# Optimization experiments

Measured on AMD Instinct MI355X. Metric: run time of the kernel, lower is better.

Reference implementation:

```python
import jax, jax.numpy as jnp
import numpy as np


def _gru(x, h, Wx, Wh, b):
    # Keras-convention GRUCell (reset_after=False): h' = z*h + (1-z)*hh
    D = h.shape[-1]
    g = x @ Wx + b                       # [N, 3D]
    xz, xr, xh = g[..., :D], g[..., D:2 * D], g[..., 2 * D:]
    z = jax.nn.sigmoid(xz + h @ Wh[:, :D])
    r = jax.nn.sigmoid(xr + h @ Wh[:, D:2 * D])
    hh = jnp.tanh(xh + (r * h) @ Wh[:, 2 * D:])
    return z * h + (1.0 - z) * hh


def setup_inputs():
    key = jax.random.key(0)
    ks = jax.random.split(key, 12)
    num_links, num_quests, num_paths = 20000, 200, 100
    total_paths = num_quests * num_paths
    L, link_dim, path_dim, T = 8, 64, 64, 8
    s = 0.05
    links = jax.random.randint(ks[0], (total_paths * L,), 0, num_links)
    paths = jnp.repeat(jnp.arange(total_paths), L)   # sorted, as segment_sum requires
    seqs = jnp.tile(jnp.arange(L), total_paths)      # hop position within each path
    return {
        "link_capacity": jax.random.uniform(ks[1], (num_links,), jnp.float32),
        "traffic": jax.random.uniform(ks[2], (total_paths,), jnp.float32),
        "links": links, "paths": paths, "seqs": seqs,
        "pWx": jax.random.normal(ks[3], (link_dim, 3 * path_dim), jnp.float32) * s,
        "pWh": jax.random.normal(ks[4], (path_dim, 3 * path_dim), jnp.float32) * s,
        "pb": jnp.zeros((3 * path_dim,), jnp.float32),
        "eWx": jax.random.normal(ks[5], (path_dim, 3 * link_dim), jnp.float32) * s,
        "eWh": jax.random.normal(ks[6], (link_dim, 3 * link_dim), jnp.float32) * s,
        "eb": jnp.zeros((3 * link_dim,), jnp.float32),
        "W1": jax.random.normal(ks[7], (path_dim, 256), jnp.float32) * s,
        "b1": jnp.zeros((256,), jnp.float32),
        "W2": jax.random.normal(ks[8], (256, 256), jnp.float32) * s,
        "b2": jnp.zeros((256,), jnp.float32),
        "W3": jax.random.normal(ks[9], (256, 1), jnp.float32) * s,
        "b3": jnp.zeros((1,), jnp.float32),
        "T": T, "num_quests": num_quests, "num_paths": num_paths,
    }


def reference(link_capacity, traffic, links, paths, seqs,
              pWx, pWh, pb, eWx, eWh, eb, W1, b1, W2, b2, W3, b3,
              T, num_quests, num_paths):
    num_links = link_capacity.shape[0]
    total_paths = num_quests * num_paths
    link_dim = eWh.shape[0]
    path_dim = pWh.shape[0]
    E = links.shape[0]
    L = E // total_paths                      # static max path length (fixed-length paths)

    # per-path lengths (tf.math.segment_sum of ones over sorted `paths`)
    lens = jax.ops.segment_sum(jnp.ones_like(paths), paths, num_segments=total_paths)

    link_state = jnp.concatenate(
        [link_capacity[:, None], jnp.zeros((num_links, link_dim - 1), link_capacity.dtype)], axis=1)
    path_state = jnp.concatenate(
        [traffic[:total_paths, None], jnp.zeros((total_paths, path_dim - 1), traffic.dtype)], axis=1)

    for _ in range(T):
        h_tild = link_state[links]                                     # gather: [E, link_dim]
        link_inputs = jnp.zeros((total_paths, L, link_dim), h_tild.dtype)
        link_inputs = link_inputs.at[paths, seqs].set(h_tild)          # scatter_nd
        xs = jnp.transpose(link_inputs, (1, 0, 2))                     # [L, P, link_dim]

        def step(h, xt):
            x, t = xt
            mask = (t < lens)[:, None]
            h_new = _gru(x, h, pWx, pWh, pb)
            h = jnp.where(mask, h_new, h)                              # freeze past seq end
            out = jnp.where(mask, h, jnp.zeros_like(h))                # dynamic_rnn zeros tail
            return h, out

        path_state, outputs = jax.lax.scan(step, path_state, (xs, jnp.arange(L)))
        m = outputs[seqs, paths]                                       # gather_nd: [E, path_dim]
        m = jax.ops.segment_sum(m, links, num_segments=num_links)      # unsorted_segment_sum
        link_state = _gru(m, link_state, eWx, eWh, eb)                 # edge GRU update

    # readout (module calls it with training=True -> dropout active; fixed masks here)
    k1, k2 = jax.random.split(jax.random.key(1))
    h = jax.nn.selu(path_state @ W1 + b1)
    h = jnp.where(jax.random.bernoulli(k1, 0.5, h.shape), h / 0.5, 0.0)
    h = jax.nn.selu(h @ W2 + b2)
    h = jnp.where(jax.random.bernoulli(k2, 0.5, h.shape), h / 0.5, 0.0)
    r = jax.nn.relu(h @ W3 + b3)
    return r.reshape(num_quests, num_paths)
```

## Files before the change

kernel.cpp:

```cpp
#include <hip/hip_runtime.h>
#include <cstdint>

#define NLINKS 20000
#define NPATHS 20000
#define LSEQ   8
#define TITER  8
#define DD     64
#define GW     192
#define NEDGE  (NPATHS * LSEQ)
#define NB     ((NPATHS + 63) / 64)

__device__ static inline void softbar() {
  asm volatile("s_waitcnt lgkmcnt(0)" ::: "memory");
  __builtin_amdgcn_s_barrier();
  asm volatile("" ::: "memory");
}

__host__ __device__ static inline uint32_t rotl32(uint32_t x, unsigned r) {
  return (x << r) | (x >> (32u - r));
}

__host__ __device__ static inline void threefry2x32(uint32_t k0, uint32_t k1,
                                                    uint32_t c0, uint32_t c1,
                                                    uint32_t& o0, uint32_t& o1) {
  uint32_t ks0 = k0, ks1 = k1, ks2 = k0 ^ k1 ^ 0x1BD11BDAu;
  uint32_t x0 = c0 + ks0, x1 = c1 + ks1;
#define TF_R(r) { x0 += x1; x1 = rotl32(x1, r); x1 ^= x0; }
  TF_R(13) TF_R(15) TF_R(26) TF_R(6)  x0 += ks1; x1 += ks2 + 1u;
  TF_R(17) TF_R(29) TF_R(16) TF_R(24) x0 += ks2; x1 += ks0 + 2u;
  TF_R(13) TF_R(15) TF_R(26) TF_R(6)  x0 += ks0; x1 += ks1 + 3u;
  TF_R(17) TF_R(29) TF_R(16) TF_R(24) x0 += ks1; x1 += ks2 + 4u;
  TF_R(13) TF_R(15) TF_R(26) TF_R(6)  x0 += ks2; x1 += ks0 + 5u;
#undef TF_R
  o0 = x0; o1 = x1;
}

__device__ static inline bool bern_keep(uint32_t key0, uint32_t key1, uint32_t j) {
  uint32_t o0, o1;
  threefry2x32(key0, key1, 0u, j, o0, o1);
  uint32_t bits = o0 ^ o1;
  float u = __uint_as_float((bits >> 9) | 0x3f800000u) - 1.0f;
  return u < 0.5f;
}

__device__ static inline float sigmoidf_(float x) { return 1.0f / (1.0f + expf(-x)); }
__device__ static inline float seluf_(float x) {
  const float sc = 1.0507009873554805f;
  const float al = 1.6732632423543772f;
  return x > 0.0f ? sc * x : sc * al * expm1f(x);
}

__global__ void init_gather_kernel(const float* __restrict__ cap,
                                   const float* __restrict__ traffic,
                                   float* __restrict__ link_state,
                                   float* __restrict__ seq_h,
                                   int* __restrict__ counts) {
  int i = blockIdx.x * blockDim.x + threadIdx.x;
  if (i < NLINKS * DD)
    link_state[i] = ((i & 63) == 0) ? cap[i >> 6] : 0.0f;
  if (i < NPATHS * DD) {
    int p = i >> 6, j = i & 63;
    seq_h[(p * LSEQ + (LSEQ - 1)) * DD + j] = (j == 0) ? traffic[p] : 0.0f;
  }
  if (i < NLINKS) counts[i] = 0;
}

__global__ void csr_hist_kernel(const int* __restrict__ links,
                                int* __restrict__ counts) {
  int e = blockIdx.x * blockDim.x + threadIdx.x;
  if (e < NEDGE) atomicAdd(&counts[links[e]], 1);
}

__global__ __launch_bounds__(1024, 1) void csr_scan_kernel(
    const int* __restrict__ counts,
    int* __restrict__ row_start,
    int* __restrict__ cursor) {
  __shared__ int sc[1024];
  const int i = threadIdx.x;
  const int base = i * 20;
  int s = 0;
  for (int j = 0; j < 20; ++j) {
    int r = base + j;
    if (r < NLINKS) s += counts[r];
  }
  sc[i] = s;
  __syncthreads();
  for (int off = 1; off < 1024; off <<= 1) {
    int v = (i >= off) ? sc[i - off] : 0;
    __syncthreads();
    sc[i] += v;
    __syncthreads();
  }
  int run = sc[i] - s;
  for (int j = 0; j < 20; ++j) {
    int r = base + j;
    if (r < NLINKS) {
      row_start[r] = run;
      cursor[r] = run;
      run += counts[r];
    }
  }
}

__global__ void csr_fill_kernel(const int* __restrict__ links,
                                int* __restrict__ cursor,
                                int* __restrict__ edges) {
  int e = blockIdx.x * blockDim.x + threadIdx.x;
  if (e < NEDGE) {
    int l = links[e];
    int pos = atomicAdd(&cursor[l], 1);
    edges[pos] = e;
  }
}

__global__ __launch_bounds__(512, 4) void gx_kernel(
    const float* __restrict__ link_state,
    const float* __restrict__ Wx,
    const float* __restrict__ bias,
    float* __restrict__ gx) {
  __shared__ float ls_s[64][65];

  const int tid  = threadIdx.x;
  const int lane = tid & 63;
  const int w    = __builtin_amdgcn_readfirstlane(tid >> 6);
  const int l0   = blockIdx.x * 64;

  for (int i = tid; i < 1024; i += 512) {
    int p = i >> 4, c = i & 15;
    int lr = min(l0 + p, NLINKS - 1);
    float4 v = reinterpret_cast<const float4*>(link_state)[lr * 16 + c];
    ls_s[p][c * 4 + 0] = v.x; ls_s[p][c * 4 + 1] = v.y;
    ls_s[p][c * 4 + 2] = v.z; ls_s[p][c * 4 + 3] = v.w;
  }

  const int c0 = w * 24;
  float acc[24];
#pragma unroll
  for (int jj = 0; jj < 24; ++jj) acc[jj] = bias[c0 + jj];
  softbar();

#pragma unroll 4
  for (int k = 0; k < DD; ++k) {
    float xk = ls_s[lane][k];
    const float* wxp = &Wx[k * GW + c0];
#pragma unroll
    for (int jj = 0; jj < 24; ++jj)
      acc[jj] = fmaf(xk, wxp[jj], acc[jj]);
  }

  if (l0 + lane < NLINKS) {
    float* dst = &gx[(size_t)(l0 + lane) * GW + c0];
#pragma unroll
    for (int s = 0; s < 6; ++s) {
      float4 v = make_float4(acc[s * 4 + 0], acc[s * 4 + 1],
                             acc[s * 4 + 2], acc[s * 4 + 3]);
      reinterpret_cast<float4*>(dst)[s] = v;
    }
  }
}

__global__ __launch_bounds__(1024, 8) void path_gru_v9_kernel(
    const float* __restrict__ gx,
    float* __restrict__ seq_h,
    const int* __restrict__ links,
    const float* __restrict__ Wh) {
  __shared__ float h_s[64][65];
  __shared__ float z_s[64][65];
  __shared__ float r_s[64][65];

  const int tid  = threadIdx.x;
  const int lane = tid & 63;
  const int w    = __builtin_amdgcn_readfirstlane(tid >> 6);
  const int p0   = blockIdx.x * 64;

  {
    int p = tid >> 4, c = tid & 15;
    int pr = min(p0 + p, NPATHS - 1);
    float4 v = reinterpret_cast<const float4*>(seq_h)[(pr * LSEQ + 7) * 16 + c];
    h_s[p][c * 4 + 0] = v.x; h_s[p][c * 4 + 1] = v.y;
    h_s[p][c * 4 + 2] = v.z; h_s[p][c * 4 + 3] = v.w;
  }

  const int ab0 = w * 8;
  const int cc0 = 128 + w * 4;
  const int hc0 = w * 4;
  const int prow = min(p0 + lane, NPATHS - 1);
  const float4* gx4 = reinterpret_cast<const float4*>(gx);

  float4 gz0, gz1, gc0;
  {
    int li = links[prow * LSEQ + 0];
    const float4* g = gx4 + (size_t)li * (GW / 4);
    gz0 = g[ab0 / 4]; gz1 = g[ab0 / 4 + 1]; gc0 = g[cc0 / 4];
  }
  softbar();

  for (int t = 0; t < LSEQ; ++t) {
    if (t > 0) {
      int p = tid >> 4, c = tid & 15;
      if (p0 + p < NPATHS) {
        float4 v = make_float4(h_s[p][c * 4 + 0], h_s[p][c * 4 + 1],
                               h_s[p][c * 4 + 2], h_s[p][c * 4 + 3]);
        reinterpret_cast<float4*>(seq_h)[((p0 + p) * LSEQ + (t - 1)) * 16 + c] = v;
      }
    }

    float aB[8];
#pragma unroll
    for (int jj = 0; jj < 8; ++jj) aB[jj] = 0.0f;
#pragma unroll 4
    for (int k = 0; k < DD; ++k) {
      float hk = h_s[lane][k];
      const float* whp = &Wh[k * GW + ab0];
#pragma unroll
      for (int jj = 0; jj < 8; ++jj)
        aB[jj] = fmaf(hk, whp[jj], aB[jj]);
    }

    float gzf[8] = {gz0.x, gz0.y, gz0.z, gz0.w, gz1.x, gz1.y, gz1.z, gz1.w};
    if (w < 8) {
#pragma unroll
      for (int jj = 0; jj < 8; ++jj)
        z_s[lane][ab0 + jj] = sigmoidf_(gzf[jj] + aB[jj]);
    } else {
#pragma unroll
      for (int jj = 0; jj < 8; ++jj) {
        int hj = ab0 - 64 + jj;
        float r = sigmoidf_(gzf[jj] + aB[jj]);
        r_s[lane][hj] = r * h_s[lane][hj];
      }
    }
    softbar();

    int li_n = (t < LSEQ - 1) ? links[prow * LSEQ + t + 1] : 0;

    float aC[4];
#pragma unroll
    for (int jj = 0; jj < 4; ++jj) aC[jj] = 0.0f;
#pragma unroll 4
    for (int k = 0; k < DD; ++k) {
      float rhk = r_s[lane][k];
      const float* whc = &Wh[k * GW + cc0];
#pragma unroll
      for (int jj = 0; jj < 4; ++jj)
        aC[jj] = fmaf(rhk, whc[jj], aC[jj]);
    }
    float gcf[4] = {gc0.x, gc0.y, gc0.z, gc0.w};
#pragma unroll
    for (int jj = 0; jj < 4; ++jj) {
      int j = hc0 + jj;
      float z    = z_s[lane][j];
      float hold = h_s[lane][j];
      float hh = tanhf(gcf[jj] + aC[jj]);
      h_s[lane][j] = z * hold + (1.0f - z) * hh;
    }

    if (t < LSEQ - 1) {
      const float4* g = gx4 + (size_t)li_n * (GW / 4);
      gz0 = g[ab0 / 4]; gz1 = g[ab0 / 4 + 1]; gc0 = g[cc0 / 4];
    }
    softbar();
  }

  {
    int p = tid >> 4, c = tid & 15;
    if (p0 + p < NPATHS) {
      float4 v = make_float4(h_s[p][c * 4 + 0], h_s[p][c * 4 + 1],
                             h_s[p][c * 4 + 2], h_s[p][c * 4 + 3]);
      reinterpret_cast<float4*>(seq_h)[((p0 + p) * LSEQ + 7) * 16 + c] = v;
    }
  }
}

__global__ __launch_bounds__(1024, 8) void link_gru_v9_kernel(
    float* __restrict__ link_state,
    const float* __restrict__ seq_h,
    const int* __restrict__ row_start,
    const int* __restrict__ row_end,
    const int* __restrict__ edges,
    const float* __restrict__ Wx,
    const float* __restrict__ Wh,
    const float* __restrict__ bias) {
  __shared__ float h_s[64][65];
  __shared__ float x_s[64][65];
  __shared__ float r_s[64][65];

  const int tid  = threadIdx.x;
  const int lane = tid & 63;
  const int w    = __builtin_amdgcn_readfirstlane(tid >> 6);
  const int l0   = blockIdx.x * 64;

  {
    int p = tid >> 4, c = tid & 15;
    float4 hv = make_float4(0.f, 0.f, 0.f, 0.f);
    float4 xv = make_float4(0.f, 0.f, 0.f, 0.f);
    if (l0 + p < NLINKS) {
      hv = reinterpret_cast<const float4*>(link_state)[(l0 + p) * 16 + c];
      const float4* s4 = reinterpret_cast<const float4*>(seq_h);
      int rs = row_start[l0 + p], re = row_end[l0 + p];
      int ii = rs;
      for (; ii + 4 <= re; ii += 4) {
        int e0 = edges[ii + 0], e1 = edges[ii + 1];
        int e2 = edges[ii + 2], e3 = edges[ii + 3];
        float4 v0 = s4[e0 * 16 + c], v1 = s4[e1 * 16 + c];
        float4 v2 = s4[e2 * 16 + c], v3 = s4[e3 * 16 + c];
        xv.x += v0.x + v1.x + v2.x + v3.x;
        xv.y += v0.y + v1.y + v2.y + v3.y;
        xv.z += v0.z + v1.z + v2.z + v3.z;
        xv.w += v0.w + v1.w + v2.w + v3.w;
      }
      for (; ii < re; ++ii) {
        int e = edges[ii];
        float4 v = s4[e * 16 + c];
        xv.x += v.x; xv.y += v.y; xv.z += v.z; xv.w += v.w;
      }
    }
    h_s[p][c * 4 + 0] = hv.x; h_s[p][c * 4 + 1] = hv.y;
    h_s[p][c * 4 + 2] = hv.z; h_s[p][c * 4 + 3] = hv.w;
    x_s[p][c * 4 + 0] = xv.x; x_s[p][c * 4 + 1] = xv.y;
    x_s[p][c * 4 + 2] = xv.z; x_s[p][c * 4 + 3] = xv.w;
  }

  const int ab0 = w * 8;
  const int cc0 = 128 + w * 4;
  const int hc0 = w * 4;

  float bab[8], bcc[4];
#pragma unroll
  for (int jj = 0; jj < 8; ++jj) bab[jj] = bias[ab0 + jj];
#pragma unroll
  for (int jj = 0; jj < 4; ++jj) bcc[jj] = bias[cc0 + jj];

  softbar();

  float aA[8], aB[8], cA[4];
#pragma unroll
  for (int jj = 0; jj < 8; ++jj) { aA[jj] = bab[jj]; aB[jj] = 0.0f; }
#pragma unroll
  for (int jj = 0; jj < 4; ++jj) cA[jj] = bcc[jj];
#pragma unroll 4
  for (int k = 0; k < DD; ++k) {
    float xk = x_s[lane][k];
    float hk = h_s[lane][k];
    const float* wxp = &Wx[k * GW + ab0];
    const float* whp = &Wh[k * GW + ab0];
    const float* wxc = &Wx[k * GW + cc0];
#pragma unroll
    for (int jj = 0; jj < 8; ++jj) {
      aA[jj] = fmaf(xk, wxp[jj], aA[jj]);
      aB[jj] = fmaf(hk, whp[jj], aB[jj]);
    }
#pragma unroll
    for (int jj = 0; jj < 4; ++jj)
      cA[jj] = fmaf(xk, wxc[jj], cA[jj]);
  }
  softbar();

  if (w < 8) {
#pragma unroll
    for (int jj = 0; jj < 8; ++jj)
      x_s[lane][ab0 + jj] = sigmoidf_(aA[jj] + aB[jj]);
  } else {
#pragma unroll
    for (int jj = 0; jj < 8; ++jj) {
      int hj = ab0 - 64 + jj;
      float r = sigmoidf_(aA[jj] + aB[jj]);
      r_s[lane][hj] = r * h_s[lane][hj];
    }
  }
  softbar();

  float aC[4];
#pragma unroll
  for (int jj = 0; jj < 4; ++jj) aC[jj] = 0.0f;
#pragma unroll 4
  for (int k = 0; k < DD; ++k) {
    float rhk = r_s[lane][k];
    const float* whc = &Wh[k * GW + cc0];
#pragma unroll
    for (int jj = 0; jj < 4; ++jj)
      aC[jj] = fmaf(rhk, whc[jj], aC[jj]);
  }
  if (l0 + lane < NLINKS) {
    float4 o;
    float* ov = &o.x;
#pragma unroll
    for (int jj = 0; jj < 4; ++jj) {
      int j = hc0 + jj;
      float z    = x_s[lane][j];
      float hold = h_s[lane][j];
      float hh = tanhf(cA[jj] + aC[jj]);
      ov[jj] = z * hold + (1.0f - z) * hh;
    }
    reinterpret_cast<float4*>(&link_state[(size_t)(l0 + lane) * DD + hc0])[0] = o;
  }
}

__global__ __launch_bounds__(1024, 1) void mlp_v8_kernel(
    const float4* __restrict__ ps4, int rs4,
    const float* __restrict__ W1, const float* __restrict__ b1,
    const float* __restrict__ W2, const float* __restrict__ b2,
    const float* __restrict__ W3, const float* __restrict__ b3,
    float* __restrict__ out,
    uint32_t k1a, uint32_t k1b, uint32_t k2a, uint32_t k2b) {
  __shared__ float ps_s[64][65];
  __shared__ float hbuf[64][257];
  __shared__ float part_s[64][17];

  const int tid  = threadIdx.x;
  const int lane = tid & 63;
  const int w    = __builtin_amdgcn_readfirstlane(tid >> 6);
  const int p0   = blockIdx.x * 64;
  const int c0   = w * 16;

  {
    int p = tid >> 4, c = tid & 15;
    int pr = min(p0 + p, NPATHS - 1);
    float4 v = ps4[(size_t)pr * rs4 + c];
    ps_s[p][c * 4 + 0] = v.x; ps_s[p][c * 4 + 1] = v.y;
    ps_s[p][c * 4 + 2] = v.z; ps_s[p][c * 4 + 3] = v.w;
  }

  float acc[16];
#pragma unroll
  for (int j = 0; j < 16; ++j) acc[j] = b1[c0 + j];
  softbar();

  const uint32_t base = (uint32_t)(p0 + lane) * 256u + (uint32_t)c0;

#pragma unroll 2
  for (int k = 0; k < DD; ++k) {
    float pk = ps_s[lane][k];
    const float* wp = &W1[k * 256 + c0];
#pragma unroll
    for (int j = 0; j < 16; ++j) acc[j] = fmaf(pk, wp[j], acc[j]);
  }
#pragma unroll
  for (int j = 0; j < 16; ++j) {
    float v = seluf_(acc[j]);
    bool keep = bern_keep(k1a, k1b, base + (uint32_t)j);
    hbuf[lane][c0 + j] = keep ? v * 2.0f : 0.0f;
  }
  softbar();

#pragma unroll
  for (int j = 0; j < 16; ++j) acc[j] = b2[c0 + j];
#pragma unroll 2
  for (int k = 0; k < 256; ++k) {
    float hk = hbuf[lane][k];
    const float* wp = &W2[k * 256 + c0];
#pragma unroll
    for (int j = 0; j < 16; ++j) acc[j] = fmaf(hk, wp[j], acc[j]);
  }

  {
    float s = 0.0f;
#pragma unroll
    for (int j = 0; j < 16; ++j) {
      float v = seluf_(acc[j]);
      bool keep = bern_keep(k2a, k2b, base + (uint32_t)j);
      float h2 = keep ? v * 2.0f : 0.0f;
      s = fmaf(h2, W3[c0 + j], s);
    }
    part_s[lane][w] = s;
  }
  softbar();

  if (w == 0) {
    float t = b3[0];
#pragma unroll
    for (int ww = 0; ww < 16; ++ww) t += part_s[lane][ww];
    if (p0 + lane < NPATHS) out[p0 + lane] = t > 0.0f ? t : 0.0f;
  }
}

extern "C" void kernel_launch(void* const* d_in, const int* in_sizes, int n_in,
                              void* d_out, int out_size, void* d_ws, size_t ws_size,
                              hipStream_t stream) {
  const float* cap     = (const float*)d_in[0];
  const float* traffic = (const float*)d_in[1];
  const int*   links   = (const int*)d_in[2];
  const float* pWx = (const float*)d_in[5];
  const float* pWh = (const float*)d_in[6];
  const float* pb  = (const float*)d_in[7];
  const float* eWx = (const float*)d_in[8];
  const float* eWh = (const float*)d_in[9];
  const float* eb  = (const float*)d_in[10];
  const float* W1  = (const float*)d_in[11];
  const float* b1  = (const float*)d_in[12];
  const float* W2  = (const float*)d_in[13];
  const float* b2  = (const float*)d_in[14];
  const float* W3  = (const float*)d_in[15];
  const float* b3  = (const float*)d_in[16];
  float* out = (float*)d_out;

  uint32_t k1a, k1b, k2a, k2b;
  threefry2x32(0u, 1u, 0u, 0u, k1a, k1b);
  threefry2x32(0u, 1u, 0u, 1u, k2a, k2b);

  const size_t n_link = (size_t)NLINKS * DD;
  const size_t n_seq  = (size_t)NPATHS * LSEQ * DD;
  const size_t n_gx   = (size_t)NLINKS * GW;

  float* link_state = (float*)d_ws;
  float* seq_h      = link_state + n_link;
  float* gx         = seq_h + n_seq;
  int*   counts     = (int*)(gx + n_gx);
  int*   row_start  = counts + NLINKS;
  int*   cursor     = row_start + NLINKS;
  int*   edges      = cursor + NLINKS;

  init_gather_kernel<<<(NLINKS * DD + 255) / 256, 256, 0, stream>>>(
      cap, traffic, link_state, seq_h, counts);
  csr_hist_kernel<<<(NEDGE + 255) / 256, 256, 0, stream>>>(links, counts);
  csr_scan_kernel<<<1, 1024, 0, stream>>>(counts, row_start, cursor);
  csr_fill_kernel<<<(NEDGE + 255) / 256, 256, 0, stream>>>(links, cursor, edges);

  for (int it = 0; it < TITER; ++it) {
    gx_kernel<<<NB, 512, 0, stream>>>(link_state, pWx, pb, gx);
    path_gru_v9_kernel<<<NB, 1024, 0, stream>>>(gx, seq_h, links, pWh);
    link_gru_v9_kernel<<<NB, 1024, 0, stream>>>(link_state, seq_h,
                                                row_start, cursor, edges,
                                                eWx, eWh, eb);
  }
  mlp_v8_kernel<<<NB, 1024, 0, stream>>>(
      (const float4*)seq_h + 7 * 16, LSEQ * 16,
      W1, b1, W2, b2, W3, b3, out, k1a, k1b, k2a, k2b);
}
```

Measured before the change: 1.451 ms.

## Fuse path input projection into link GRU kernel and shrink MLP shared memory

The per-iteration gx projection (link_state @ pWx + pb) moves into the tail of the link GRU kernel, using the freshly computed link state kept in shared memory. This drops one kernel launch per iteration and avoids re-reading link_state from global memory. The MLP kernel reuses a single shared buffer for its input and hidden activations, with an extra barrier, and uses deeper unrolling. The fused kernel does more work per block and adds a barrier, which may lengthen the link GRU kernel. The final iteration also computes a gx that is never used.

```diff
diff --git a/kernel.cpp b/kernel.cpp
--- a/kernel.cpp
+++ b/kernel.cpp
@@ -272,7 +272,7 @@
   }
 }
 
-__global__ __launch_bounds__(1024, 8) void link_gru_v9_kernel(
+__global__ __launch_bounds__(1024, 8) void link_gru_v11_kernel(
     float* __restrict__ link_state,
     const float* __restrict__ seq_h,
     const int* __restrict__ row_start,
@@ -280,7 +280,10 @@
     const int* __restrict__ edges,
     const float* __restrict__ Wx,
     const float* __restrict__ Wh,
-    const float* __restrict__ bias) {
+    const float* __restrict__ bias,
+    const float* __restrict__ pWx,
+    const float* __restrict__ pb,
+    float* __restrict__ gx_out) {
   __shared__ float h_s[64][65];
   __shared__ float x_s[64][65];
   __shared__ float r_s[64][65];
@@ -381,30 +384,55 @@
     for (int jj = 0; jj < 4; ++jj)
       aC[jj] = fmaf(rhk, whc[jj], aC[jj]);
   }
-  if (l0 + lane < NLINKS) {
-    float4 o;
-    float* ov = &o.x;
+  {
+    float o[4];
 #pragma unroll
     for (int jj = 0; jj < 4; ++jj) {
       int j = hc0 + jj;
       float z    = x_s[lane][j];
       float hold = h_s[lane][j];
       float hh = tanhf(cA[jj] + aC[jj]);
-      ov[jj] = z * hold + (1.0f - z) * hh;
-    }
-    reinterpret_cast<float4*>(&link_state[(size_t)(l0 + lane) * DD + hc0])[0] = o;
-  }
-}
-
-__global__ __launch_bounds__(1024, 1) void mlp_v8_kernel(
+      o[jj] = z * hold + (1.0f - z) * hh;
+      x_s[lane][j] = o[jj];
+    }
+    if (l0 + lane < NLINKS) {
+      reinterpret_cast<float4*>(&link_state[(size_t)(l0 + lane) * DD + hc0])[0]
+          = make_float4(o[0], o[1], o[2], o[3]);
+    }
+  }
+  softbar();
+
+  {
+    const int g0 = w * 12;
+    float ga[12];
+#pragma unroll
+    for (int jj = 0; jj < 12; ++jj) ga[jj] = pb[g0 + jj];
+#pragma unroll 4
+    for (int k = 0; k < DD; ++k) {
+      float hk = x_s[lane][k];
+      const float* wxp = &pWx[k * GW + g0];
+#pragma unroll
+      for (int jj = 0; jj < 12; ++jj)
+        ga[jj] = fmaf(hk, wxp[jj], ga[jj]);
+    }
+    if (l0 + lane < NLINKS) {
+      float* dst = &gx_out[(size_t)(l0 + lane) * GW + g0];
+#pragma unroll
+      for (int s = 0; s < 3; ++s)
+        reinterpret_cast<float4*>(dst)[s] =
+            make_float4(ga[s * 4 + 0], ga[s * 4 + 1], ga[s * 4 + 2], ga[s * 4 + 3]);
+    }
+  }
+}
+
+__global__ __launch_bounds__(1024, 8) void mlp_v9_kernel(
     const float4* __restrict__ ps4, int rs4,
     const float* __restrict__ W1, const float* __restrict__ b1,
     const float* __restrict__ W2, const float* __restrict__ b2,
     const float* __restrict__ W3, const float* __restrict__ b3,
     float* __restrict__ out,
     uint32_t k1a, uint32_t k1b, uint32_t k2a, uint32_t k2b) {
-  __shared__ float ps_s[64][65];
-  __shared__ float hbuf[64][257];
+  __shared__ float hraw[64 * 257];
   __shared__ float part_s[64][17];
 
   const int tid  = threadIdx.x;
@@ -417,8 +445,8 @@
     int p = tid >> 4, c = tid & 15;
     int pr = min(p0 + p, NPATHS - 1);
     float4 v = ps4[(size_t)pr * rs4 + c];
-    ps_s[p][c * 4 + 0] = v.x; ps_s[p][c * 4 + 1] = v.y;
-    ps_s[p][c * 4 + 2] = v.z; ps_s[p][c * 4 + 3] = v.w;
+    hraw[p * 65 + c * 4 + 0] = v.x; hraw[p * 65 + c * 4 + 1] = v.y;
+    hraw[p * 65 + c * 4 + 2] = v.z; hraw[p * 65 + c * 4 + 3] = v.w;
   }
 
   float acc[16];
@@ -428,26 +456,28 @@
 
   const uint32_t base = (uint32_t)(p0 + lane) * 256u + (uint32_t)c0;
 
-#pragma unroll 2
+#pragma unroll 4
   for (int k = 0; k < DD; ++k) {
-    float pk = ps_s[lane][k];
+    float pk = hraw[lane * 65 + k];
     const float* wp = &W1[k * 256 + c0];
 #pragma unroll
     for (int j = 0; j < 16; ++j) acc[j] = fmaf(pk, wp[j], acc[j]);
   }
+  softbar();
+
 #pragma unroll
   for (int j = 0; j < 16; ++j) {
     float v = seluf_(acc[j]);
     bool keep = bern_keep(k1a, k1b, base + (uint32_t)j);
-    hbuf[lane][c0 + j] = keep ? v * 2.0f : 0.0f;
+    hraw[lane * 257 + c0 + j] = keep ? v * 2.0f : 0.0f;
   }
   softbar();
 
 #pragma unroll
   for (int j = 0; j < 16; ++j) acc[j] = b2[c0 + j];
-#pragma unroll 2
+#pragma unroll 4
   for (int k = 0; k < 256; ++k) {
-    float hk = hbuf[lane][k];
+    float hk = hraw[lane * 257 + k];
     const float* wp = &W2[k * 256 + c0];
 #pragma unroll
     for (int j = 0; j < 16; ++j) acc[j] = fmaf(hk, wp[j], acc[j]);
@@ -516,14 +546,16 @@
   csr_scan_kernel<<<1, 1024, 0, stream>>>(counts, row_start, cursor);
   csr_fill_kernel<<<(NEDGE + 255) / 256, 256, 0, stream>>>(links, cursor, edges);
 
+  gx_kernel<<<NB, 512, 0, stream>>>(link_state, pWx, pb, gx);
+
   for (int it = 0; it < TITER; ++it) {
-    gx_kernel<<<NB, 512, 0, stream>>>(link_state, pWx, pb, gx);
     path_gru_v9_kernel<<<NB, 1024, 0, stream>>>(gx, seq_h, links, pWh);
-    link_gru_v9_kernel<<<NB, 1024, 0, stream>>>(link_state, seq_h,
-                                                row_start, cursor, edges,
-                                                eWx, eWh, eb);
-  }
-  mlp_v8_kernel<<<NB, 1024, 0, stream>>>(
+    link_gru_v11_kernel<<<NB, 1024, 0, stream>>>(link_state, seq_h,
+                                                 row_start, cursor, edges,
+                                                 eWx, eWh, eb,
+                                                 pWx, pb, gx);
+  }
+  mlp_v9_kernel<<<NB, 1024, 0, stream>>>(
       (const float4*)seq_h + 7 * 16, LSEQ * 16,
       W1, b1, W2, b2, W3, b3, out, k1a, k1b, k2a, k2b);
 }
```

Result: no change. 1.450 ms (-0.0%).
